# Kernel tuning notes

Measured on AMD Instinct MI355X. Metric: run time of the kernel, lower is better.

Reference implementation:

```python
import jax, jax.numpy as jnp
import numpy as np

N = 20000   # nodes
E = 160000  # edges
G = 32      # graphs in the batch
IN_DIM, HID, OUT = 27, 512, 256


def _linear_init(key, fan_in, fan_out):
    s = 1.0 / np.sqrt(fan_in)
    return jax.random.uniform(key, (fan_in, fan_out), jnp.float32, -s, s)


def setup_inputs() -> dict:
    key = jax.random.key(0)
    ks = jax.random.split(key, 16)
    feature = jax.random.normal(ks[0], (N, IN_DIM), jnp.float32)
    edge_src = jax.random.randint(ks[1], (E,), 0, N, jnp.int32)
    edge_dst = jax.random.randint(ks[2], (E,), 0, N, jnp.int32)
    graph_ids = jnp.sort(jax.random.randint(ks[3], (N,), 0, G, jnp.int32))
    dims = [(IN_DIM, HID), (HID, HID), (HID, OUT)]
    inp = {
        "feature": feature,
        "edge_src": edge_src,
        "edge_dst": edge_dst,
        "graph_ids": graph_ids,
    }
    k = 4
    for l, (fi, fo) in enumerate(dims):
        inp[f"W_self{l}"] = _linear_init(ks[k], fi, fo); k += 1
        inp[f"W_neigh{l}"] = _linear_init(ks[k], fi, fo); k += 1
        inp[f"b{l}"] = jnp.zeros((fo,), jnp.float32)
    return inp


def _sage_layer(h, edge_src, edge_dst, inv_deg, W_self, W_neigh, b):
    # mean aggregation of in-neighbors (src -> dst), DGL SAGEConv 'mean'
    msg = h[edge_src]                                   # [E, F]
    agg = jax.ops.segment_sum(msg, edge_dst, num_segments=N) * inv_deg  # [N, F]
    return h @ W_self + agg @ W_neigh + b


def reference(feature, edge_src, edge_dst, graph_ids,
              W_self0, W_neigh0, b0,
              W_self1, W_neigh1, b1,
              W_self2, W_neigh2, b2):
    ones_e = jnp.ones((E,), jnp.float32)
    deg = jax.ops.segment_sum(ones_e, edge_dst, num_segments=N)
    inv_deg = (1.0 / jnp.maximum(deg, 1.0))[:, None]    # [N, 1]

    h = _sage_layer(feature, edge_src, edge_dst, inv_deg, W_self0, W_neigh0, b0)
    h = jax.nn.relu(h)
    h = _sage_layer(h, edge_src, edge_dst, inv_deg, W_self1, W_neigh1, b1)
    h = jax.nn.relu(h)
    h = _sage_layer(h, edge_src, edge_dst, inv_deg, W_self2, W_neigh2, b2)
    # last layer: no activation (encoding=False -> last_activation=None)

    # AvgPooling: per-graph mean of node features
    ones_n = jnp.ones((N,), jnp.float32)
    counts = jax.ops.segment_sum(ones_n, graph_ids, num_segments=G)
    hg = jax.ops.segment_sum(h, graph_ids, num_segments=G) / jnp.maximum(counts, 1.0)[:, None]
    return h, hg
```

## Files before the change

kernel.cpp:

```cpp
#include <hip/hip_runtime.h>

constexpr int NN   = 20000;
constexpr int NE   = 160000;
constexpr int NG   = 32;
constexpr int IN   = 27;
constexpr int HID  = 512;
constexpr int OUT  = 256;
constexpr int MPAD = 20096;
constexpr int MT64 = MPAD / 64;

typedef unsigned short u16;
typedef __bf16 bf16x8 __attribute__((ext_vector_type(8)));
typedef float  f32x4  __attribute__((ext_vector_type(4)));
typedef u16    u16x4  __attribute__((ext_vector_type(4)));

__device__ __forceinline__ u16 f2b(float x) {
  __bf16 h = (__bf16)x;
  return __builtin_bit_cast(u16, h);
}
__device__ __forceinline__ float b2f(u16 u) {
  __bf16 h = __builtin_bit_cast(__bf16, u);
  return (float)h;
}

#define GLOBAL_AS __attribute__((address_space(1)))
#define LDS_AS    __attribute__((address_space(3)))
__device__ __forceinline__ void gload_lds16(const void* g, void* l) {
  __builtin_amdgcn_global_load_lds((const GLOBAL_AS void*)g, (LDS_AS void*)l, 16, 0, 0);
}

__global__ void k_deg(const int* __restrict__ dst, int* __restrict__ deg) {
  int e = blockIdx.x * 256 + threadIdx.x;
  if (e < NE) atomicAdd(&deg[dst[e]], 1);
}

__global__ void k_scan(const int* __restrict__ deg, int* __restrict__ rowptr,
                       int* __restrict__ cursor, float* __restrict__ invdeg) {
  constexpr int CH = 20;
  __shared__ int sdeg[1024 * CH];
  __shared__ int wsum[16];
  const int tid = threadIdx.x;
  for (int j = tid; j < 1024 * CH; j += 1024) sdeg[j] = (j < NN) ? deg[j] : 0;
  __syncthreads();
  const int i0 = tid * CH;
  int loc[CH];
  int sum = 0;
#pragma unroll
  for (int j = 0; j < CH; ++j) { loc[j] = sum; sum += sdeg[i0 + j]; }
  const int lane = tid & 63, wv = tid >> 6;
  int incl = sum;
#pragma unroll
  for (int off = 1; off < 64; off <<= 1) {
    int n = __shfl_up(incl, off);
    if (lane >= off) incl += n;
  }
  if (lane == 63) wsum[wv] = incl;
  __syncthreads();
  if (tid == 0) {
    int s = 0;
#pragma unroll
    for (int w = 0; w < 16; ++w) { int v = wsum[w]; wsum[w] = s + v; s += v; }
  }
  __syncthreads();
  const int wbase = (wv == 0) ? 0 : wsum[wv - 1];
  const int tbase = wbase + incl - sum;
#pragma unroll
  for (int j = 0; j < CH; ++j) {
    const int i = i0 + j;
    if (i < NN) {
      const int excl = tbase + loc[j];
      const int d = sdeg[i];
      rowptr[i] = excl;
      cursor[i] = excl;
      invdeg[i] = 1.0f / fmaxf((float)d, 1.0f);
    }
  }
  if (tid == 0) rowptr[NN] = wsum[15];
}

__global__ void k_scatter(const int* __restrict__ src, const int* __restrict__ dst,
                          int* __restrict__ cursor, int* __restrict__ ssrc) {
  int e = blockIdx.x * 256 + threadIdx.x;
  if (e < NE) {
    int p = atomicAdd(&cursor[dst[e]], 1);
    ssrc[p] = src[e];
  }
}

constexpr int WC0 = 512 * 64;
constexpr int WC1 = 512 * 1024;
constexpr int WC2 = 256 * 1024;
constexpr int WCT = WC0 + WC1 + WC2;
__global__ void k_wconv_all(const float* __restrict__ Ws0, const float* __restrict__ Wn0,
                            const float* __restrict__ Ws1, const float* __restrict__ Wn1,
                            const float* __restrict__ Ws2, const float* __restrict__ Wn2,
                            u16* __restrict__ Bt0, u16* __restrict__ Bt1,
                            u16* __restrict__ BtSN2) {
  int idx = blockIdx.x * 256 + threadIdx.x;
  if (idx < WC0) {
    const int n = idx / 64, k = idx % 64;
    float v = 0.0f;
    if (k < IN)           v = Ws0[(size_t)k * 512 + n];
    else if (k < 2 * IN)  v = Wn0[(size_t)(k - IN) * 512 + n];
    Bt0[idx] = f2b(v);
    return;
  }
  idx -= WC0;
  if (idx < WC1) {
    const int n = idx / 1024, k = idx % 1024;
    const float v = (k < 512) ? Ws1[(size_t)k * 512 + n] : Wn1[(size_t)(k - 512) * 512 + n];
    Bt1[idx] = f2b(v);
    return;
  }
  idx -= WC1;
  if (idx < WC2) {
    const int n = idx / 1024, k = idx % 1024;
    const float v = (k < 512) ? Ws2[(size_t)k * 256 + n] : Wn2[(size_t)(k - 512) * 256 + n];
    BtSN2[idx] = f2b(v);
  }
}

__global__ void k_build_A0(const float* __restrict__ feat, const int* __restrict__ rowptr,
                           const int* __restrict__ ssrc, const float* __restrict__ invdeg,
                           u16* __restrict__ A0) {
  const int r = blockIdx.x, t = threadIdx.x;
  u16* row = A0 + (size_t)r * 64;
  if (r >= NN) { row[t] = 0; return; }
  if (t < IN) {
    row[t] = f2b(feat[(size_t)r * IN + t]);
    float s = 0.0f;
    const int e0 = rowptr[r], e1 = rowptr[r + 1];
    for (int e = e0; e < e1; ++e) s += feat[(size_t)ssrc[e] * IN + t];
    row[IN + t] = f2b(s * invdeg[r]);
  } else if (t >= 2 * IN) {
    row[t] = 0;
  }
}

__global__ void k_agg512(u16* __restrict__ X, const int* __restrict__ rowptr,
                         const int* __restrict__ ssrc, const float* __restrict__ invdeg) {
  const int r = blockIdx.x, t = threadIdx.x;
  float a0 = 0, a1 = 0, a2 = 0, a3 = 0;
  const int e0 = rowptr[r], e1 = rowptr[r + 1];
  for (int e = e0; e < e1; ++e) {
    const u16x4 v = *(const u16x4*)(X + (size_t)ssrc[e] * 1024 + t * 4);
    a0 += b2f(v.x); a1 += b2f(v.y); a2 += b2f(v.z); a3 += b2f(v.w);
  }
  const float inv = invdeg[r];
  u16x4 o; o.x = f2b(a0 * inv); o.y = f2b(a1 * inv); o.z = f2b(a2 * inv); o.w = f2b(a3 * inv);
  *(u16x4*)(X + (size_t)r * 1024 + 512 + t * 4) = o;
}

__global__ __launch_bounds__(256, 6) void k_gemm(
    const u16* __restrict__ A, int lda,
    const u16* __restrict__ Bt, int K,
    void* __restrict__ Out, int ldo,
    const float* __restrict__ bias,
    int flags, int nt) {
  __shared__ u16 As[64 * 64];
  __shared__ u16 Bs[128 * 64];
  const int tid = threadIdx.x;
  const int wid = tid >> 6, lane = tid & 63;
  const int l16 = lane & 15, lhi = lane >> 4;
  const int wr = wid >> 1, wc = wid & 1;

  const int G    = gridDim.x;
  const int PER  = nt * 8;
  const int nOct = G / PER;
  const int base = nOct * PER;
  int x, y;
  if ((int)blockIdx.x < base) {
    x = (blockIdx.x & 7) + 8 * (blockIdx.x / PER);
    y = (blockIdx.x >> 3) & (nt - 1);
  } else {
    const int j = blockIdx.x - base;
    x = 8 * nOct + j / nt;
    y = j - (j / nt) * nt;
  }
  const int row0 = x * 64, col0 = y * 128;

  f32x4 acc[2][4] = {};

  for (int kt = 0; kt < K; kt += 64) {
#pragma unroll
    for (int p = 0; p < 2; ++p) {
      const int o = tid + p * 256;
      const int r = o >> 3, sl = o & 7;
      const int ss = sl ^ (r & 7);
      gload_lds16(A + (size_t)(row0 + r) * lda + kt + ss * 8,
                  &As[(wid * 64 + p * 256) * 8]);
    }
#pragma unroll
    for (int p = 0; p < 4; ++p) {
      const int o = tid + p * 256;
      const int r = o >> 3, sl = o & 7;
      const int ss = sl ^ (r & 7);
      gload_lds16(Bt + (size_t)(col0 + r) * K + kt + ss * 8,
                  &Bs[(wid * 64 + p * 256) * 8]);
    }
    __syncthreads();
#pragma unroll
    for (int ks = 0; ks < 2; ++ks) {
      bf16x8 af[2], bfr[4];
#pragma unroll
      for (int i = 0; i < 2; ++i) {
        const int r = wr * 32 + i * 16 + l16;
        const int s = (ks * 4 + lhi) ^ (r & 7);
        af[i] = *(const bf16x8*)&As[r * 64 + s * 8];
      }
#pragma unroll
      for (int n = 0; n < 4; ++n) {
        const int c = wc * 64 + n * 16 + l16;
        const int s = (ks * 4 + lhi) ^ (c & 7);
        bfr[n] = *(const bf16x8*)&Bs[c * 64 + s * 8];
      }
#pragma unroll
      for (int i = 0; i < 2; ++i)
#pragma unroll
        for (int n = 0; n < 4; ++n)
          acc[i][n] = __builtin_amdgcn_mfma_f32_16x16x32_bf16(af[i], bfr[n], acc[i][n], 0, 0, 0);
    }
    __syncthreads();
  }

  const bool relu = flags & 1;
  const bool f32o = flags & 2;
#pragma unroll
  for (int i = 0; i < 2; ++i) {
#pragma unroll
    for (int n = 0; n < 4; ++n) {
      const int C = col0 + wc * 64 + n * 16 + l16;
      const float bv = bias ? bias[C] : 0.0f;
#pragma unroll
      for (int q = 0; q < 4; ++q) {
        const int R = row0 + wr * 32 + i * 16 + lhi * 4 + q;
        float v = acc[i][n][q] + bv;
        if (f32o) {
          if (R < NN) ((float*)Out)[(size_t)R * ldo + C] = v;
        } else {
          if (relu) v = fmaxf(v, 0.0f);
          ((u16*)Out)[(size_t)R * ldo + C] = f2b(v);
        }
      }
    }
  }
}

__device__ __forceinline__ int lower_bound_g(const int* __restrict__ gid, int g) {
  int lo = 0, hi = NN;
  while (lo < hi) {
    const int mid = (lo + hi) >> 1;
    if (gid[mid] < g) lo = mid + 1; else hi = mid;
  }
  return lo;
}
__global__ void k_pool(const float* __restrict__ h, const int* __restrict__ gid,
                       float* __restrict__ hg) {
  __shared__ int s_n0, s_n1;
  const int g = blockIdx.x >> 3, s = blockIdx.x & 7;
  const int t = threadIdx.x;
  if (t == 0) { s_n0 = lower_bound_g(gid, g); s_n1 = lower_bound_g(gid, g + 1); }
  __syncthreads();
  const int n0 = s_n0, n1 = s_n1;
  const int len = n1 - n0, chunk = (len + 7) / 8;
  const int a = n0 + s * chunk;
  const int b = min(a + chunk, n1);
  float acc = 0.0f;
  for (int i = a; i < b; ++i) acc += h[(size_t)i * 256 + t];
  if (b > a) {
    const float inv = 1.0f / fmaxf((float)len, 1.0f);
    atomicAdd(&hg[g * 256 + t], acc * inv);
  }
}

constexpr size_t OFF_A0    = 0;
constexpr size_t OFF_A1    = OFF_A0   + (size_t)MPAD * 64  * 2;
constexpr size_t OFF_A2    = OFF_A1   + (size_t)MPAD * 1024 * 2;
constexpr size_t OFF_BT0   = OFF_A2   + (size_t)MPAD * 1024 * 2;
constexpr size_t OFF_BT1   = OFF_BT0  + (size_t)512 * 64 * 2;
constexpr size_t OFF_BTSN2 = OFF_BT1  + (size_t)512 * 1024 * 2;
constexpr size_t OFF_DEG   = OFF_BTSN2+ (size_t)256 * 1024 * 2;
constexpr size_t OFF_RP    = OFF_DEG  + (size_t)NN * 4;
constexpr size_t OFF_CUR   = OFF_RP   + (size_t)(NN + 2) * 4;
constexpr size_t OFF_SSRC  = OFF_CUR  + (size_t)NN * 4;
constexpr size_t OFF_INVD  = OFF_SSRC + (size_t)NE * 4;

extern "C" void kernel_launch(void* const* d_in, const int* in_sizes, int n_in,
                              void* d_out, int out_size, void* d_ws, size_t ws_size,
                              hipStream_t stream) {
  const float* feature = (const float*)d_in[0];
  const int*   esrc    = (const int*)d_in[1];
  const int*   edst    = (const int*)d_in[2];
  const int*   gid     = (const int*)d_in[3];
  const float* Ws0 = (const float*)d_in[4],  *Wn0 = (const float*)d_in[5],  *b0 = (const float*)d_in[6];
  const float* Ws1 = (const float*)d_in[7],  *Wn1 = (const float*)d_in[8],  *b1 = (const float*)d_in[9];
  const float* Ws2 = (const float*)d_in[10], *Wn2 = (const float*)d_in[11], *b2 = (const float*)d_in[12];

  char* ws = (char*)d_ws;
  u16*   A0    = (u16*)  (ws + OFF_A0);
  u16*   A1    = (u16*)  (ws + OFF_A1);
  u16*   A2    = (u16*)  (ws + OFF_A2);
  u16*   Bt0   = (u16*)  (ws + OFF_BT0);
  u16*   Bt1   = (u16*)  (ws + OFF_BT1);
  u16*   BtSN2 = (u16*)  (ws + OFF_BTSN2);
  int*   deg   = (int*)  (ws + OFF_DEG);
  int*   rp    = (int*)  (ws + OFF_RP);
  int*   cur   = (int*)  (ws + OFF_CUR);
  int*   ssrc  = (int*)  (ws + OFF_SSRC);
  float* invd  = (float*)(ws + OFF_INVD);

  float* out_h  = (float*)d_out;
  float* out_hg = out_h + (size_t)NN * OUT;

  hipMemsetAsync(deg,  0, (size_t)NN * 4, stream);
  hipMemsetAsync(out_hg, 0, (size_t)NG * OUT * 4, stream);

  k_deg    <<<(NE + 255) / 256, 256, 0, stream>>>(edst, deg);
  k_scan   <<<1, 1024, 0, stream>>>(deg, rp, cur, invd);
  k_scatter<<<(NE + 255) / 256, 256, 0, stream>>>(esrc, edst, cur, ssrc);

  k_wconv_all<<<(WCT + 255) / 256, 256, 0, stream>>>(Ws0, Wn0, Ws1, Wn1, Ws2, Wn2,
                                                     Bt0, Bt1, BtSN2);

  k_build_A0<<<MPAD, 64, 0, stream>>>(feature, rp, ssrc, invd, A0);
  k_gemm<<<MT64 * 4, 256, 0, stream>>>(A0, 64, Bt0, 64, A1, 1024, b0, 1, 4);

  k_agg512<<<NN, 128, 0, stream>>>(A1, rp, ssrc, invd);
  k_gemm<<<MT64 * 4, 256, 0, stream>>>(A1, 1024, Bt1, 1024, A2, 1024, b1, 1, 4);

  k_agg512<<<NN, 128, 0, stream>>>(A2, rp, ssrc, invd);
  k_gemm<<<MT64 * 2, 256, 0, stream>>>(A2, 1024, BtSN2, 1024, out_h, 256, b2, 2, 2);

  k_pool<<<NG * 8, 256, 0, stream>>>(out_h, gid, out_hg);
}
```

Baseline: 295.4 us.

## Fuse preprocessing launches, vectorize neighbor aggregation, simplify pooling

```diff
diff --git a/kernel.cpp b/kernel.cpp
--- a/kernel.cpp
+++ b/kernel.cpp
@@ -12,7 +12,7 @@
 typedef unsigned short u16;
 typedef __bf16 bf16x8 __attribute__((ext_vector_type(8)));
 typedef float  f32x4  __attribute__((ext_vector_type(4)));
-typedef u16    u16x4  __attribute__((ext_vector_type(4)));
+typedef u16    u16x8  __attribute__((ext_vector_type(8)));
 
 __device__ __forceinline__ u16 f2b(float x) {
   __bf16 h = (__bf16)x;
@@ -29,18 +29,15 @@
   __builtin_amdgcn_global_load_lds((const GLOBAL_AS void*)g, (LDS_AS void*)l, 16, 0, 0);
 }
 
-__global__ void k_deg(const int* __restrict__ dst, int* __restrict__ deg) {
-  int e = blockIdx.x * 256 + threadIdx.x;
-  if (e < NE) atomicAdd(&deg[dst[e]], 1);
-}
-
-__global__ void k_scan(const int* __restrict__ deg, int* __restrict__ rowptr,
+__global__ void k_scan(const int* __restrict__ edst, int* __restrict__ rowptr,
                        int* __restrict__ cursor, float* __restrict__ invdeg) {
   constexpr int CH = 20;
   __shared__ int sdeg[1024 * CH];
   __shared__ int wsum[16];
   const int tid = threadIdx.x;
-  for (int j = tid; j < 1024 * CH; j += 1024) sdeg[j] = (j < NN) ? deg[j] : 0;
+  for (int j = tid; j < 1024 * CH; j += 1024) sdeg[j] = 0;
+  __syncthreads();
+  for (int e = tid; e < NE; e += 1024) atomicAdd(&sdeg[edst[e]], 1);
   __syncthreads();
   const int i0 = tid * CH;
   int loc[CH];
@@ -78,25 +75,29 @@
   if (tid == 0) rowptr[NN] = wsum[15];
 }
 
-__global__ void k_scatter(const int* __restrict__ src, const int* __restrict__ dst,
-                          int* __restrict__ cursor, int* __restrict__ ssrc) {
-  int e = blockIdx.x * 256 + threadIdx.x;
-  if (e < NE) {
-    int p = atomicAdd(&cursor[dst[e]], 1);
-    ssrc[p] = src[e];
-  }
-}
-
 constexpr int WC0 = 512 * 64;
 constexpr int WC1 = 512 * 1024;
 constexpr int WC2 = 256 * 1024;
 constexpr int WCT = WC0 + WC1 + WC2;
-__global__ void k_wconv_all(const float* __restrict__ Ws0, const float* __restrict__ Wn0,
-                            const float* __restrict__ Ws1, const float* __restrict__ Wn1,
-                            const float* __restrict__ Ws2, const float* __restrict__ Wn2,
-                            u16* __restrict__ Bt0, u16* __restrict__ Bt1,
-                            u16* __restrict__ BtSN2) {
-  int idx = blockIdx.x * 256 + threadIdx.x;
+constexpr int SCT_BLK = (NE + 255) / 256;
+constexpr int WCV_BLK = (WCT + 255) / 256;
+__global__ void k_scatter_wconv(const int* __restrict__ src, const int* __restrict__ dst,
+                                int* __restrict__ cursor, int* __restrict__ ssrc,
+                                const float* __restrict__ Ws0, const float* __restrict__ Wn0,
+                                const float* __restrict__ Ws1, const float* __restrict__ Wn1,
+                                const float* __restrict__ Ws2, const float* __restrict__ Wn2,
+                                u16* __restrict__ Bt0, u16* __restrict__ Bt1,
+                                u16* __restrict__ BtSN2) {
+  const int b = blockIdx.x;
+  if (b < SCT_BLK) {
+    const int e = b * 256 + threadIdx.x;
+    if (e < NE) {
+      int p = atomicAdd(&cursor[dst[e]], 1);
+      ssrc[p] = src[e];
+    }
+    return;
+  }
+  int idx = (b - SCT_BLK) * 256 + threadIdx.x;
   if (idx < WC0) {
     const int n = idx / 64, k = idx % 64;
     float v = 0.0f;
@@ -130,7 +131,14 @@
     row[t] = f2b(feat[(size_t)r * IN + t]);
     float s = 0.0f;
     const int e0 = rowptr[r], e1 = rowptr[r + 1];
-    for (int e = e0; e < e1; ++e) s += feat[(size_t)ssrc[e] * IN + t];
+    int e = e0;
+    for (; e + 1 < e1; e += 2) {
+      const int s0 = ssrc[e], s1 = ssrc[e + 1];
+      const float f0 = feat[(size_t)s0 * IN + t];
+      const float f1 = feat[(size_t)s1 * IN + t];
+      s += f0; s += f1;
+    }
+    if (e < e1) s += feat[(size_t)ssrc[e] * IN + t];
     row[IN + t] = f2b(s * invdeg[r]);
   } else if (t >= 2 * IN) {
     row[t] = 0;
@@ -139,16 +147,29 @@
 
 __global__ void k_agg512(u16* __restrict__ X, const int* __restrict__ rowptr,
                          const int* __restrict__ ssrc, const float* __restrict__ invdeg) {
-  const int r = blockIdx.x, t = threadIdx.x;
-  float a0 = 0, a1 = 0, a2 = 0, a3 = 0;
+  const int r = blockIdx.x * 4 + (threadIdx.x >> 6);
+  if (r >= NN) return;
+  const int lane = threadIdx.x & 63;
+  float a[8] = {};
   const int e0 = rowptr[r], e1 = rowptr[r + 1];
-  for (int e = e0; e < e1; ++e) {
-    const u16x4 v = *(const u16x4*)(X + (size_t)ssrc[e] * 1024 + t * 4);
-    a0 += b2f(v.x); a1 += b2f(v.y); a2 += b2f(v.z); a3 += b2f(v.w);
+  int e = e0;
+  for (; e + 1 < e1; e += 2) {
+    const int s0 = ssrc[e], s1 = ssrc[e + 1];
+    const u16x8 v0 = *(const u16x8*)(X + (size_t)s0 * 1024 + lane * 8);
+    const u16x8 v1 = *(const u16x8*)(X + (size_t)s1 * 1024 + lane * 8);
+#pragma unroll
+    for (int j = 0; j < 8; ++j) { a[j] += b2f(v0[j]); a[j] += b2f(v1[j]); }
+  }
+  if (e < e1) {
+    const u16x8 v0 = *(const u16x8*)(X + (size_t)ssrc[e] * 1024 + lane * 8);
+#pragma unroll
+    for (int j = 0; j < 8; ++j) a[j] += b2f(v0[j]);
   }
   const float inv = invdeg[r];
-  u16x4 o; o.x = f2b(a0 * inv); o.y = f2b(a1 * inv); o.z = f2b(a2 * inv); o.w = f2b(a3 * inv);
-  *(u16x4*)(X + (size_t)r * 1024 + 512 + t * 4) = o;
+  u16x8 o;
+#pragma unroll
+  for (int j = 0; j < 8; ++j) o[j] = f2b(a[j] * inv);
+  *(u16x8*)(X + (size_t)r * 1024 + 512 + lane * 8) = o;
 }
 
 __global__ __launch_bounds__(256, 6) void k_gemm(
@@ -257,20 +278,14 @@
 __global__ void k_pool(const float* __restrict__ h, const int* __restrict__ gid,
                        float* __restrict__ hg) {
   __shared__ int s_n0, s_n1;
-  const int g = blockIdx.x >> 3, s = blockIdx.x & 7;
+  const int g = blockIdx.x;
   const int t = threadIdx.x;
   if (t == 0) { s_n0 = lower_bound_g(gid, g); s_n1 = lower_bound_g(gid, g + 1); }
   __syncthreads();
   const int n0 = s_n0, n1 = s_n1;
-  const int len = n1 - n0, chunk = (len + 7) / 8;
-  const int a = n0 + s * chunk;
-  const int b = min(a + chunk, n1);
   float acc = 0.0f;
-  for (int i = a; i < b; ++i) acc += h[(size_t)i * 256 + t];
-  if (b > a) {
-    const float inv = 1.0f / fmaxf((float)len, 1.0f);
-    atomicAdd(&hg[g * 256 + t], acc * inv);
-  }
+  for (int i = n0; i < n1; ++i) acc += h[(size_t)i * 256 + t];
+  hg[g * 256 + t] = acc / fmaxf((float)(n1 - n0), 1.0f);
 }
 
 constexpr size_t OFF_A0    = 0;
@@ -279,8 +294,7 @@
 constexpr size_t OFF_BT0   = OFF_A2   + (size_t)MPAD * 1024 * 2;
 constexpr size_t OFF_BT1   = OFF_BT0  + (size_t)512 * 64 * 2;
 constexpr size_t OFF_BTSN2 = OFF_BT1  + (size_t)512 * 1024 * 2;
-constexpr size_t OFF_DEG   = OFF_BTSN2+ (size_t)256 * 1024 * 2;
-constexpr size_t OFF_RP    = OFF_DEG  + (size_t)NN * 4;
+constexpr size_t OFF_RP    = OFF_BTSN2+ (size_t)256 * 1024 * 2;
 constexpr size_t OFF_CUR   = OFF_RP   + (size_t)(NN + 2) * 4;
 constexpr size_t OFF_SSRC  = OFF_CUR  + (size_t)NN * 4;
 constexpr size_t OFF_INVD  = OFF_SSRC + (size_t)NE * 4;
@@ -303,7 +317,6 @@
   u16*   Bt0   = (u16*)  (ws + OFF_BT0);
   u16*   Bt1   = (u16*)  (ws + OFF_BT1);
   u16*   BtSN2 = (u16*)  (ws + OFF_BTSN2);
-  int*   deg   = (int*)  (ws + OFF_DEG);
   int*   rp    = (int*)  (ws + OFF_RP);
   int*   cur   = (int*)  (ws + OFF_CUR);
   int*   ssrc  = (int*)  (ws + OFF_SSRC);
@@ -312,24 +325,18 @@
   float* out_h  = (float*)d_out;
   float* out_hg = out_h + (size_t)NN * OUT;
 
-  hipMemsetAsync(deg,  0, (size_t)NN * 4, stream);
-  hipMemsetAsync(out_hg, 0, (size_t)NG * OUT * 4, stream);
-
-  k_deg    <<<(NE + 255) / 256, 256, 0, stream>>>(edst, deg);
-  k_scan   <<<1, 1024, 0, stream>>>(deg, rp, cur, invd);
-  k_scatter<<<(NE + 255) / 256, 256, 0, stream>>>(esrc, edst, cur, ssrc);
-
-  k_wconv_all<<<(WCT + 255) / 256, 256, 0, stream>>>(Ws0, Wn0, Ws1, Wn1, Ws2, Wn2,
-                                                     Bt0, Bt1, BtSN2);
+  k_scan<<<1, 1024, 0, stream>>>(edst, rp, cur, invd);
+  k_scatter_wconv<<<SCT_BLK + WCV_BLK, 256, 0, stream>>>(
+      esrc, edst, cur, ssrc, Ws0, Wn0, Ws1, Wn1, Ws2, Wn2, Bt0, Bt1, BtSN2);
 
   k_build_A0<<<MPAD, 64, 0, stream>>>(feature, rp, ssrc, invd, A0);
   k_gemm<<<MT64 * 4, 256, 0, stream>>>(A0, 64, Bt0, 64, A1, 1024, b0, 1, 4);
 
-  k_agg512<<<NN, 128, 0, stream>>>(A1, rp, ssrc, invd);
+  k_agg512<<<(NN + 3) / 4, 256, 0, stream>>>(A1, rp, ssrc, invd);
   k_gemm<<<MT64 * 4, 256, 0, stream>>>(A1, 1024, Bt1, 1024, A2, 1024, b1, 1, 4);
 
-  k_agg512<<<NN, 128, 0, stream>>>(A2, rp, ssrc, invd);
+  k_agg512<<<(NN + 3) / 4, 256, 0, stream>>>(A2, rp, ssrc, invd);
   k_gemm<<<MT64 * 2, 256, 0, stream>>>(A2, 1024, BtSN2, 1024, out_h, 256, b2, 2, 2);
 
-  k_pool<<<NG * 8, 256, 0, stream>>>(out_h, gid, out_hg);
-}
+  k_pool<<<NG, 256, 0, stream>>>(out_h, gid, out_hg);
+}
```

After: 434.8 us. 47.2% more time.
